# Performance work log

Hardware: AMD Instinct MI355X
Metric: run time of the kernel (lower is better)

Reference implementation:

```python
import jax, jax.numpy as jnp
import numpy as np

N_NODES = 10000
N_EDGES = 160000
IN_DIM = 512
HID_DIM = 512
OUT_DIM = 256
N_CLASSES = 8
N_GRAPHS = 64


def gcn_conv(x, W, b, src, dst, n):
    # PyG GCNConv: x @ W, add self-loops, symmetric normalization, scatter-add, + bias
    h = x @ W  # [N, out]
    loops = jnp.arange(n, dtype=src.dtype)
    src2 = jnp.concatenate([src, loops])
    dst2 = jnp.concatenate([dst, loops])
    deg = jax.ops.segment_sum(jnp.ones(src2.shape[0], h.dtype), dst2, num_segments=n)
    dinv = jnp.where(deg > 0, jax.lax.rsqrt(deg), 0.0)
    norm = dinv[src2] * dinv[dst2]          # [E+N]
    msgs = h[src2] * norm[:, None]          # gather + weight
    out = jax.ops.segment_sum(msgs, dst2, num_segments=n)  # scatter-add
    return out + b


def setup_inputs() -> dict:
    key = jax.random.key(0)
    ks = jax.random.split(key, 10)
    x = jax.random.normal(ks[0], (N_NODES, IN_DIM), dtype=jnp.float32)
    edge_index = jax.random.randint(ks[1], (2, N_EDGES), 0, N_NODES, dtype=jnp.int64)
    batch = jnp.sort(jax.random.randint(ks[2], (N_NODES,), 0, N_GRAPHS, dtype=jnp.int64))
    s = 0.02
    W1 = jax.random.normal(ks[3], (IN_DIM, HID_DIM), dtype=jnp.float32) * s
    b1 = jnp.zeros((HID_DIM,), jnp.float32)
    W2 = jax.random.normal(ks[4], (HID_DIM, OUT_DIM), dtype=jnp.float32) * s
    b2 = jnp.zeros((OUT_DIM,), jnp.float32)
    Wl = jax.random.normal(ks[5], (OUT_DIM, N_CLASSES), dtype=jnp.float32) * s
    bl = jnp.zeros((N_CLASSES,), jnp.float32)
    return {"x": x, "W1": W1, "b1": b1, "W2": W2, "b2": b2,
            "Wl": Wl, "bl": bl, "edge_index": edge_index, "batch": batch}


def reference(x, W1, b1, W2, b2, Wl, bl, edge_index, batch):
    src, dst = edge_index[0], edge_index[1]
    h = jax.nn.relu(gcn_conv(x, W1, b1, src, dst, N_NODES))
    # dropout(p=0.5) is identity at inference (training=False)
    h = jax.nn.relu(gcn_conv(h, W2, b2, src, dst, N_NODES))
    # global_mean_pool over graph ids
    sums = jax.ops.segment_sum(h, batch, num_segments=N_GRAPHS)
    cnts = jax.ops.segment_sum(jnp.ones((N_NODES,), h.dtype), batch, num_segments=N_GRAPHS)
    pooled = sums / jnp.maximum(cnts, 1.0)[:, None]  # [G, OUT_DIM]
    return pooled @ Wl + bl
```

## Files before the change

kernel.cpp:

```cpp
#include <hip/hip_runtime.h>

#define N_NODES   10000
#define IN_DIM    512
#define HID_DIM   512
#define OUT_DIM   256
#define N_CLASSES 8
#define N_GRAPHS  64

typedef __attribute__((ext_vector_type(8))) __bf16 bf16x8;
typedef __attribute__((ext_vector_type(4))) float f32x4;
typedef __attribute__((ext_vector_type(8))) unsigned short ushort8;
typedef __attribute__((ext_vector_type(4))) unsigned short ushort4v;

__device__ __forceinline__ unsigned short f2bf(float f) {
    union { float f; unsigned int u; } v; v.f = f;
    unsigned int r = v.u + 0x7FFFu + ((v.u >> 16) & 1u);
    return (unsigned short)(r >> 16);
}
__device__ __forceinline__ float bf2f(unsigned short u) {
    union { unsigned int u; float f; } v; v.u = ((unsigned int)u) << 16;
    return v.f;
}

__global__ void count_deg_kernel(const int* __restrict__ dst, int* __restrict__ cnt, int E) {
    int e = blockIdx.x * blockDim.x + threadIdx.x;
    if (e < E) atomicAdd(&cnt[dst[e]], 1);
}

__global__ __launch_bounds__(1024) void scan_prep_kernel(const int* __restrict__ cnt,
                                                         int* __restrict__ offs,
                                                         int* __restrict__ pos,
                                                         float* __restrict__ dinv,
                                                         const int* __restrict__ batch,
                                                         int* __restrict__ start, int n) {
    __shared__ int partial[1024];
    int tid = threadIdx.x;
    const int CH = (n + 1023) >> 10;
    int base = tid * CH;
    int s = 0;
    for (int i = 0; i < CH; i++) { int idx = base + i; if (idx < n) s += cnt[idx]; }
    partial[tid] = s;
    __syncthreads();
    for (int off = 1; off < 1024; off <<= 1) {
        int v = (tid >= off) ? partial[tid - off] : 0;
        __syncthreads();
        partial[tid] += v;
        __syncthreads();
    }
    int run = (tid > 0) ? partial[tid - 1] : 0;
    for (int i = 0; i < CH; i++) {
        int idx = base + i;
        if (idx < n) {
            int c = cnt[idx];
            offs[idx] = run; pos[idx] = run; run += c;
            dinv[idx] = rsqrtf((float)(c + 1));
            int b  = batch[idx];
            int bn = (idx + 1 < n) ? batch[idx + 1] : N_GRAPHS;
            for (int g = b + 1; g <= bn; g++) start[g] = idx + 1;
            if (idx == 0) for (int g = 0; g <= b; g++) start[g] = 0;
        }
    }
    if (tid == 0) offs[n] = partial[1023];
}

__global__ void fill_csr_kernel(const int* __restrict__ src, const int* __restrict__ dst,
                                const float* __restrict__ dinv, int* __restrict__ pos,
                                int* __restrict__ csrs, float* __restrict__ csrn, int E) {
    int e = blockIdx.x * blockDim.x + threadIdx.x;
    if (e < E) {
        int s = src[e], d = dst[e];
        int p = atomicAdd(&pos[d], 1);
        csrs[p] = s;
        csrn[p] = dinv[s] * dinv[d];
    }
}

__global__ __launch_bounds__(256) void cvt_all_kernel(const float* __restrict__ W1,
                                                      unsigned short* __restrict__ W1t,
                                                      const float* __restrict__ W2,
                                                      unsigned short* __restrict__ W2t,
                                                      const float* __restrict__ x,
                                                      unsigned short* __restrict__ xb, int total8) {
    int b = blockIdx.x;
    if (b < 384) {
        __shared__ float t[32][33];
        const float* W; unsigned short* Wt; int K, N, bn, bk;
        if (b < 256) { W = W1; Wt = W1t; K = IN_DIM;  N = HID_DIM; bn = (b & 15) * 32; bk = (b >> 4) * 32; }
        else { int b2 = b - 256; W = W2; Wt = W2t; K = HID_DIM; N = OUT_DIM; bn = (b2 & 7) * 32; bk = (b2 >> 3) * 32; }
        int tx = threadIdx.x & 31, ty = threadIdx.x >> 5;
        #pragma unroll
        for (int j = 0; j < 32; j += 8)
            t[ty + j][tx] = W[(size_t)(bk + ty + j) * N + bn + tx];
        __syncthreads();
        #pragma unroll
        for (int j = 0; j < 32; j += 8)
            Wt[(size_t)(bn + ty + j) * K + bk + tx] = f2bf(t[tx][ty + j]);
    } else {
        int i = (b - 384) * 256 + threadIdx.x;
        if (i < total8) {
            float4 f0 = *reinterpret_cast<const float4*>(&x[(size_t)i * 8]);
            float4 f1 = *reinterpret_cast<const float4*>(&x[(size_t)i * 8 + 4]);
            ushort8 v;
            v[0] = f2bf(f0.x); v[1] = f2bf(f0.y); v[2] = f2bf(f0.z); v[3] = f2bf(f0.w);
            v[4] = f2bf(f1.x); v[5] = f2bf(f1.y); v[6] = f2bf(f1.z); v[7] = f2bf(f1.w);
            *reinterpret_cast<ushort8*>(&xb[(size_t)i * 8]) = v;
        }
    }
}

template<int BM, int BN, bool OUT_BF16>
__global__ __launch_bounds__(256) void mfma_gemm_kernel(const unsigned short* __restrict__ A,
                                                        const unsigned short* __restrict__ Bt,
                                                        void* __restrict__ Cp,
                                                        int M, int N, int K) {
    constexpr int BK = 32, PK = 40;
    constexpr int FM = BM / 32, FN = BN / 32;
    __shared__ unsigned short As[BM * PK];
    __shared__ unsigned short Bs[BN * PK];
    int tid  = threadIdx.x;
    int lane = tid & 63;
    int wid  = tid >> 6;
    int wm = wid >> 1, wn = wid & 1;
    int row0 = blockIdx.x * BM, col0 = blockIdx.y * BN;

    f32x4 acc[FM][FN] = {};

    for (int k0 = 0; k0 < K; k0 += BK) {
        #pragma unroll
        for (int i = 0; i < BM * 4 / 256; i++) {
            int l  = tid + i * 256;
            int r  = l >> 2;
            int cg = (l & 3) << 3;
            int gr = row0 + r;
            ushort8 av = {0, 0, 0, 0, 0, 0, 0, 0};
            if (gr < M) av = *reinterpret_cast<const ushort8*>(&A[(size_t)gr * K + k0 + cg]);
            *reinterpret_cast<ushort8*>(&As[r * PK + cg]) = av;
        }
        #pragma unroll
        for (int i = 0; i < BN * 4 / 256; i++) {
            int l  = tid + i * 256;
            int r  = l >> 2;
            int cg = (l & 3) << 3;
            *reinterpret_cast<ushort8*>(&Bs[r * PK + cg]) =
                *reinterpret_cast<const ushort8*>(&Bt[(size_t)(col0 + r) * K + k0 + cg]);
        }
        __syncthreads();
        int kk = (lane >> 4) << 3;
        int ra = (wm * (BM / 2) + (lane & 15)) * PK + kk;
        int rb = (wn * (BN / 2) + (lane & 15)) * PK + kk;
        bf16x8 a[FM], b[FN];
        #pragma unroll
        for (int m = 0; m < FM; m++)
            a[m] = *reinterpret_cast<const bf16x8*>(&As[ra + m * 16 * PK]);
        #pragma unroll
        for (int nn = 0; nn < FN; nn++)
            b[nn] = *reinterpret_cast<const bf16x8*>(&Bs[rb + nn * 16 * PK]);
        #pragma unroll
        for (int m = 0; m < FM; m++)
            #pragma unroll
            for (int nn = 0; nn < FN; nn++)
                acc[m][nn] = __builtin_amdgcn_mfma_f32_16x16x32_bf16(a[m], b[nn], acc[m][nn], 0, 0, 0);
        __syncthreads();
    }

    int rbase = row0 + wm * (BM / 2) + ((lane >> 4) << 2);
    int cbase = col0 + wn * (BN / 2) + (lane & 15);
    #pragma unroll
    for (int m = 0; m < FM; m++) {
        #pragma unroll
        for (int nn = 0; nn < FN; nn++) {
            #pragma unroll
            for (int j = 0; j < 4; j++) {
                int row = rbase + m * 16 + j;
                if (row < M) {
                    int col = cbase + nn * 16;
                    if (OUT_BF16) ((unsigned short*)Cp)[(size_t)row * N + col] = f2bf(acc[m][nn][j]);
                    else          ((float*)Cp)[(size_t)row * N + col] = acc[m][nn][j];
                }
            }
        }
    }
}

__global__ __launch_bounds__(256) void agg512_kernel(const unsigned short* __restrict__ h,
                                                     const int* __restrict__ offs,
                                                     const int* __restrict__ csrs,
                                                     const float* __restrict__ csrn,
                                                     const float* __restrict__ dinv,
                                                     const float* __restrict__ bias,
                                                     unsigned short* __restrict__ outp, int n) {
    int wid = threadIdx.x >> 6, lane = threadIdx.x & 63;
    int i = blockIdx.x * 4 + wid;
    if (i >= n) return;
    int f = lane * 8;
    float di = dinv[i], w0 = di * di;
    ushort8 hv = *reinterpret_cast<const ushort8*>(&h[(size_t)i * 512 + f]);
    float acc[8];
    #pragma unroll
    for (int j = 0; j < 8; j++) acc[j] = bf2f(hv[j]) * w0;
    int p = offs[i], p1 = offs[i + 1];
    for (; p + 4 <= p1; p += 4) {
        int s0 = csrs[p], s1 = csrs[p + 1], s2 = csrs[p + 2], s3 = csrs[p + 3];
        float wa = csrn[p], wb = csrn[p + 1], wc = csrn[p + 2], wd = csrn[p + 3];
        ushort8 v0 = *reinterpret_cast<const ushort8*>(&h[(size_t)s0 * 512 + f]);
        ushort8 v1 = *reinterpret_cast<const ushort8*>(&h[(size_t)s1 * 512 + f]);
        ushort8 v2 = *reinterpret_cast<const ushort8*>(&h[(size_t)s2 * 512 + f]);
        ushort8 v3 = *reinterpret_cast<const ushort8*>(&h[(size_t)s3 * 512 + f]);
        #pragma unroll
        for (int j = 0; j < 8; j++) {
            acc[j] = fmaf(wa, bf2f(v0[j]), acc[j]);
            acc[j] = fmaf(wb, bf2f(v1[j]), acc[j]);
            acc[j] = fmaf(wc, bf2f(v2[j]), acc[j]);
            acc[j] = fmaf(wd, bf2f(v3[j]), acc[j]);
        }
    }
    for (; p < p1; p++) {
        int s = csrs[p]; float w = csrn[p];
        ushort8 v = *reinterpret_cast<const ushort8*>(&h[(size_t)s * 512 + f]);
        #pragma unroll
        for (int j = 0; j < 8; j++) acc[j] = fmaf(w, bf2f(v[j]), acc[j]);
    }
    float4 b0 = *reinterpret_cast<const float4*>(&bias[f]);
    float4 b1 = *reinterpret_cast<const float4*>(&bias[f + 4]);
    ushort8 r;
    r[0] = f2bf(fmaxf(acc[0] + b0.x, 0.f)); r[1] = f2bf(fmaxf(acc[1] + b0.y, 0.f));
    r[2] = f2bf(fmaxf(acc[2] + b0.z, 0.f)); r[3] = f2bf(fmaxf(acc[3] + b0.w, 0.f));
    r[4] = f2bf(fmaxf(acc[4] + b1.x, 0.f)); r[5] = f2bf(fmaxf(acc[5] + b1.y, 0.f));
    r[6] = f2bf(fmaxf(acc[6] + b1.z, 0.f)); r[7] = f2bf(fmaxf(acc[7] + b1.w, 0.f));
    *reinterpret_cast<ushort8*>(&outp[(size_t)i * 512 + f]) = r;
}

__global__ __launch_bounds__(256) void agg256_kernel(const unsigned short* __restrict__ h,
                                                     const int* __restrict__ offs,
                                                     const int* __restrict__ csrs,
                                                     const float* __restrict__ csrn,
                                                     const float* __restrict__ dinv,
                                                     const float* __restrict__ bias,
                                                     unsigned short* __restrict__ outp, int n) {
    int wid = threadIdx.x >> 6, lane = threadIdx.x & 63;
    int i = blockIdx.x * 4 + wid;
    if (i >= n) return;
    int f = lane * 4;
    float di = dinv[i], w0 = di * di;
    ushort4v hv = *reinterpret_cast<const ushort4v*>(&h[(size_t)i * 256 + f]);
    float acc[4];
    #pragma unroll
    for (int j = 0; j < 4; j++) acc[j] = bf2f(hv[j]) * w0;
    int p = offs[i], p1 = offs[i + 1];
    for (; p + 4 <= p1; p += 4) {
        int s0 = csrs[p], s1 = csrs[p + 1], s2 = csrs[p + 2], s3 = csrs[p + 3];
        float wa = csrn[p], wb = csrn[p + 1], wc = csrn[p + 2], wd = csrn[p + 3];
        ushort4v v0 = *reinterpret_cast<const ushort4v*>(&h[(size_t)s0 * 256 + f]);
        ushort4v v1 = *reinterpret_cast<const ushort4v*>(&h[(size_t)s1 * 256 + f]);
        ushort4v v2 = *reinterpret_cast<const ushort4v*>(&h[(size_t)s2 * 256 + f]);
        ushort4v v3 = *reinterpret_cast<const ushort4v*>(&h[(size_t)s3 * 256 + f]);
        #pragma unroll
        for (int j = 0; j < 4; j++) {
            acc[j] = fmaf(wa, bf2f(v0[j]), acc[j]);
            acc[j] = fmaf(wb, bf2f(v1[j]), acc[j]);
            acc[j] = fmaf(wc, bf2f(v2[j]), acc[j]);
            acc[j] = fmaf(wd, bf2f(v3[j]), acc[j]);
        }
    }
    for (; p < p1; p++) {
        int s = csrs[p]; float w = csrn[p];
        ushort4v v = *reinterpret_cast<const ushort4v*>(&h[(size_t)s * 256 + f]);
        #pragma unroll
        for (int j = 0; j < 4; j++) acc[j] = fmaf(w, bf2f(v[j]), acc[j]);
    }
    float4 bv = *reinterpret_cast<const float4*>(&bias[f]);
    ushort4v r;
    r[0] = f2bf(fmaxf(acc[0] + bv.x, 0.f)); r[1] = f2bf(fmaxf(acc[1] + bv.y, 0.f));
    r[2] = f2bf(fmaxf(acc[2] + bv.z, 0.f)); r[3] = f2bf(fmaxf(acc[3] + bv.w, 0.f));
    *reinterpret_cast<ushort4v*>(&outp[(size_t)i * 256 + f]) = r;
}

__global__ __launch_bounds__(256) void pool_head_kernel(const unsigned short* __restrict__ agg2b,
                                                        const int* __restrict__ start,
                                                        const float* __restrict__ Wl,
                                                        const float* __restrict__ bl,
                                                        float* __restrict__ out) {
    __shared__ float smem[8][OUT_DIM];
    int g = blockIdx.x;
    int t = threadIdx.x;
    int ry = t >> 5;
    int cg = (t & 31) << 3;
    int s0 = start[g], s1 = start[g + 1];
    float acc[8] = {};
    for (int r = s0 + ry; r < s1; r += 8) {
        ushort8 v = *reinterpret_cast<const ushort8*>(&agg2b[(size_t)r * OUT_DIM + cg]);
        #pragma unroll
        for (int j = 0; j < 8; j++) acc[j] += bf2f(v[j]);
    }
    #pragma unroll
    for (int j = 0; j < 8; j++) smem[ry][cg + j] = acc[j];
    __syncthreads();
    float inv = 1.0f / fmaxf((float)(s1 - s0), 1.0f);
    float s = 0.f;
    #pragma unroll
    for (int r2 = 0; r2 < 8; r2++) s += smem[r2][t];
    float pooled_t = s * inv;
    __syncthreads();
    smem[0][t] = pooled_t;
    __syncthreads();
    int c = t >> 5, j = t & 31;
    float part = 0.f;
    #pragma unroll
    for (int m = 0; m < 8; m++) {
        int k = j + m * 32;
        part = fmaf(smem[0][k], Wl[k * N_CLASSES + c], part);
    }
    #pragma unroll
    for (int m = 16; m >= 1; m >>= 1) part += __shfl_xor(part, m, 32);
    if (j == 0) out[g * N_CLASSES + c] = part + bl[c];
}

extern "C" void kernel_launch(void* const* d_in, const int* in_sizes, int n_in,
                              void* d_out, int out_size, void* d_ws, size_t ws_size,
                              hipStream_t stream) {
    const float* x   = (const float*)d_in[0];
    const float* W1  = (const float*)d_in[1];
    const float* b1  = (const float*)d_in[2];
    const float* W2  = (const float*)d_in[3];
    const float* b2  = (const float*)d_in[4];
    const float* Wl  = (const float*)d_in[5];
    const float* bl  = (const float*)d_in[6];
    const int*   ei  = (const int*)d_in[7];
    const int*   bat = (const int*)d_in[8];
    float* out = (float*)d_out;

    const int n = N_NODES;
    const int E = in_sizes[7] / 2;
    const int* src = ei;
    const int* dst = ei + E;

    unsigned short* xb    = (unsigned short*)d_ws;
    unsigned short* h2b   = xb + (size_t)n * IN_DIM;
    unsigned short* agg2b = h2b + (size_t)n * OUT_DIM;
    unsigned short* h1b   = agg2b + (size_t)n * OUT_DIM;
    unsigned short* agg1b = h1b + (size_t)n * HID_DIM;
    unsigned short* W1t   = agg1b + (size_t)n * HID_DIM;
    unsigned short* W2t   = W1t + IN_DIM * HID_DIM;
    int*   cnt   = (int*)(W2t + HID_DIM * OUT_DIM);
    int*   offs  = cnt + n;
    int*   pos   = offs + n + 1;
    int*   csrs  = pos + n;
    float* csrn  = (float*)(csrs + E);
    float* dinv  = csrn + E;
    int*   start = (int*)(dinv + n);

    hipMemsetAsync(cnt, 0, n * sizeof(int), stream);

    count_deg_kernel<<<(E + 255) / 256, 256, 0, stream>>>(dst, cnt, E);
    scan_prep_kernel<<<1, 1024, 0, stream>>>(cnt, offs, pos, dinv, bat, start, n);
    fill_csr_kernel<<<(E + 255) / 256, 256, 0, stream>>>(src, dst, dinv, pos, csrs, csrn, E);

    int total8 = n * IN_DIM / 8;
    cvt_all_kernel<<<384 + (total8 + 255) / 256, 256, 0, stream>>>(W1, W1t, W2, W2t, x, xb, total8);

    dim3 g1((n + 127) / 128, HID_DIM / 64);
    mfma_gemm_kernel<128, 64, true><<<g1, 256, 0, stream>>>(xb, W1t, h1b, n, HID_DIM, IN_DIM);
    agg512_kernel<<<(n + 3) / 4, 256, 0, stream>>>(h1b, offs, csrs, csrn, dinv, b1, agg1b, n);

    dim3 g2((n + 127) / 128, OUT_DIM / 64);
    mfma_gemm_kernel<128, 64, true><<<g2, 256, 0, stream>>>(agg1b, W2t, h2b, n, OUT_DIM, HID_DIM);
    agg256_kernel<<<(n + 3) / 4, 256, 0, stream>>>(h2b, offs, csrs, csrn, dinv, b2, agg2b, n);

    pool_head_kernel<<<N_GRAPHS, OUT_DIM, 0, stream>>>(agg2b, start, Wl, bl, out);
}
```

Before: 212.1 us.

## Load GEMM tiles directly into LDS and widen first GEMM tile

```diff
diff --git a/kernel.cpp b/kernel.cpp
--- a/kernel.cpp
+++ b/kernel.cpp
@@ -20,6 +20,12 @@
 __device__ __forceinline__ float bf2f(unsigned short u) {
     union { unsigned int u; float f; } v; v.u = ((unsigned int)u) << 16;
     return v.f;
+}
+
+__device__ __forceinline__ void gload16(const unsigned short* g, unsigned short* l) {
+    __builtin_amdgcn_global_load_lds(
+        (const __attribute__((address_space(1))) unsigned int*)g,
+        (__attribute__((address_space(3))) unsigned int*)l, 16, 0, 0);
 }
 
 __global__ void count_deg_kernel(const int* __restrict__ dst, int* __restrict__ cnt, int E) {
@@ -108,15 +114,15 @@
     }
 }
 
-template<int BM, int BN, bool OUT_BF16>
+template<int BM, int BN>
 __global__ __launch_bounds__(256) void mfma_gemm_kernel(const unsigned short* __restrict__ A,
                                                         const unsigned short* __restrict__ Bt,
-                                                        void* __restrict__ Cp,
+                                                        unsigned short* __restrict__ C,
                                                         int M, int N, int K) {
-    constexpr int BK = 32, PK = 40;
+    constexpr int BK = 32;
     constexpr int FM = BM / 32, FN = BN / 32;
-    __shared__ unsigned short As[BM * PK];
-    __shared__ unsigned short Bs[BN * PK];
+    __shared__ unsigned short As[BM * BK];
+    __shared__ unsigned short Bs[BN * BK];
     int tid  = threadIdx.x;
     int lane = tid & 63;
     int wid  = tid >> 6;
@@ -127,34 +133,29 @@
 
     for (int k0 = 0; k0 < K; k0 += BK) {
         #pragma unroll
-        for (int i = 0; i < BM * 4 / 256; i++) {
-            int l  = tid + i * 256;
-            int r  = l >> 2;
-            int cg = (l & 3) << 3;
-            int gr = row0 + r;
-            ushort8 av = {0, 0, 0, 0, 0, 0, 0, 0};
-            if (gr < M) av = *reinterpret_cast<const ushort8*>(&A[(size_t)gr * K + k0 + cg]);
-            *reinterpret_cast<ushort8*>(&As[r * PK + cg]) = av;
-        }
-        #pragma unroll
-        for (int i = 0; i < BN * 4 / 256; i++) {
-            int l  = tid + i * 256;
-            int r  = l >> 2;
-            int cg = (l & 3) << 3;
-            *reinterpret_cast<ushort8*>(&Bs[r * PK + cg]) =
-                *reinterpret_cast<const ushort8*>(&Bt[(size_t)(col0 + r) * K + k0 + cg]);
-        }
-        __syncthreads();
+        for (int i = 0; i < BM / 64; i++) {
+            int sb = (wid * (BM / 64) + i) * 64;
+            int s  = sb + lane;
+            gload16(&A[(size_t)(row0 + (s >> 2)) * K + k0 + ((s & 3) << 3)], &As[sb * 8]);
+        }
+        #pragma unroll
+        for (int i = 0; i < BN / 64; i++) {
+            int sb = (wid * (BN / 64) + i) * 64;
+            int s  = sb + lane;
+            gload16(&Bt[(size_t)(col0 + (s >> 2)) * K + k0 + ((s & 3) << 3)], &Bs[sb * 8]);
+        }
+        __syncthreads();
+
         int kk = (lane >> 4) << 3;
-        int ra = (wm * (BM / 2) + (lane & 15)) * PK + kk;
-        int rb = (wn * (BN / 2) + (lane & 15)) * PK + kk;
+        int ra = (wm * (BM / 2) + (lane & 15)) * BK + kk;
+        int rb = (wn * (BN / 2) + (lane & 15)) * BK + kk;
         bf16x8 a[FM], b[FN];
         #pragma unroll
         for (int m = 0; m < FM; m++)
-            a[m] = *reinterpret_cast<const bf16x8*>(&As[ra + m * 16 * PK]);
+            a[m] = *reinterpret_cast<const bf16x8*>(&As[ra + m * 16 * BK]);
         #pragma unroll
         for (int nn = 0; nn < FN; nn++)
-            b[nn] = *reinterpret_cast<const bf16x8*>(&Bs[rb + nn * 16 * PK]);
+            b[nn] = *reinterpret_cast<const bf16x8*>(&Bs[rb + nn * 16 * BK]);
         #pragma unroll
         for (int m = 0; m < FM; m++)
             #pragma unroll
@@ -172,11 +173,7 @@
             #pragma unroll
             for (int j = 0; j < 4; j++) {
                 int row = rbase + m * 16 + j;
-                if (row < M) {
-                    int col = cbase + nn * 16;
-                    if (OUT_BF16) ((unsigned short*)Cp)[(size_t)row * N + col] = f2bf(acc[m][nn][j]);
-                    else          ((float*)Cp)[(size_t)row * N + col] = acc[m][nn][j];
-                }
+                if (row < M) C[(size_t)row * N + cbase + nn * 16] = f2bf(acc[m][nn][j]);
             }
         }
     }
@@ -358,12 +355,12 @@
     int total8 = n * IN_DIM / 8;
     cvt_all_kernel<<<384 + (total8 + 255) / 256, 256, 0, stream>>>(W1, W1t, W2, W2t, x, xb, total8);
 
-    dim3 g1((n + 127) / 128, HID_DIM / 64);
-    mfma_gemm_kernel<128, 64, true><<<g1, 256, 0, stream>>>(xb, W1t, h1b, n, HID_DIM, IN_DIM);
+    dim3 g1((n + 127) / 128, HID_DIM / 128);
+    mfma_gemm_kernel<128, 128><<<g1, 256, 0, stream>>>(xb, W1t, h1b, n, HID_DIM, IN_DIM);
     agg512_kernel<<<(n + 3) / 4, 256, 0, stream>>>(h1b, offs, csrs, csrn, dinv, b1, agg1b, n);
 
     dim3 g2((n + 127) / 128, OUT_DIM / 64);
-    mfma_gemm_kernel<128, 64, true><<<g2, 256, 0, stream>>>(agg1b, W2t, h2b, n, OUT_DIM, HID_DIM);
+    mfma_gemm_kernel<128, 64><<<g2, 256, 0, stream>>>(agg1b, W2t, h2b, n, OUT_DIM, HID_DIM);
     agg256_kernel<<<(n + 3) / 4, 256, 0, stream>>>(h2b, offs, csrs, csrn, dinv, b2, agg2b, n);
 
     pool_head_kernel<<<N_GRAPHS, OUT_DIM, 0, stream>>>(agg2b, start, Wl, bl, out);
```

Measured after the change: 208.9 us. Within noise of the previous version (-1.5%).
